# Kernel optimization log

Measured on AMD Instinct MI355X. Metric: run time of the kernel, lower is better.

Reference implementation:

```python
import jax, jax.numpy as jnp
import numpy as np

NUM_FILTER = 256
CAPS_LEN = 8
NUM_EMOTIONS = 8
OUT_DIM = 16
NUM_CHANNEL = 25
TIME_LEN = 25
NUM_CAPS = NUM_CHANNEL * TIME_LEN * (NUM_FILTER // CAPS_LEN)  # 20000
NUM_ITERATIONS = 3


def setup_inputs() -> dict:
    key = jax.random.key(0)
    ks = jax.random.split(key, 10)
    B = 32
    x = jax.random.normal(ks[0], (B, 54, 54), jnp.float32)
    conv1_w = jax.random.normal(ks[1], (NUM_FILTER, 1, 6, 6), jnp.float32) * 0.05
    conv1_b = jax.random.normal(ks[2], (NUM_FILTER,), jnp.float32) * 0.01
    conv2_w = jax.random.normal(ks[3], (NUM_FILTER, NUM_FILTER, 6, 6), jnp.float32) * 0.01
    conv2_b = jax.random.normal(ks[4], (NUM_FILTER,), jnp.float32) * 0.01
    conv3_w = jax.random.normal(ks[5], (NUM_FILTER, 2 * NUM_FILTER, 1, 1), jnp.float32) * 0.05
    conv3_b = jax.random.normal(ks[6], (NUM_FILTER,), jnp.float32) * 0.01
    # PrimaryCaps: one Linear(caps_len -> caps_len) per capsule, batched as [nc, out, in]
    pc_w = jax.random.normal(ks[7], (NUM_CAPS, CAPS_LEN, CAPS_LEN), jnp.float32) * 0.1
    pc_b = jax.random.normal(ks[8], (NUM_CAPS, CAPS_LEN), jnp.float32) * 0.1
    # EmotionCaps transform W: [nc, num_emotions, out_dim, in_dim]
    W = jax.random.normal(ks[9], (NUM_CAPS, NUM_EMOTIONS, OUT_DIM, CAPS_LEN), jnp.float32) * 0.05
    return {"x": x, "conv1_w": conv1_w, "conv1_b": conv1_b, "conv2_w": conv2_w,
            "conv2_b": conv2_b, "conv3_w": conv3_w, "conv3_b": conv3_b,
            "pc_w": pc_w, "pc_b": pc_b, "W": W}


def _conv(x, w, b, stride):
    y = jax.lax.conv_general_dilated(x, w, (stride, stride), 'VALID',
                                     dimension_numbers=('NCHW', 'OIHW', 'NCHW'))
    return y + b[None, :, None, None]


def _squash(s):
    # scale = |s|^2 / (1 + |s|^2); out = scale * s / (|s| + 1e-8)
    n2 = jnp.sum(s * s, axis=-1, keepdims=True)
    n = jnp.sqrt(n2)
    return (n2 / (1.0 + n2)) * s / (n + 1e-8)


def reference(x, conv1_w, conv1_b, conv2_w, conv2_b, conv3_w, conv3_b, pc_w, pc_b, W):
    x4 = x[:, None]                                    # [B,1,54,54]
    x1 = jax.nn.relu(_conv(x4, conv1_w, conv1_b, 2))   # [B,F,25,25]
    y = jnp.pad(x1, ((0, 0), (0, 0), (2, 3), (2, 3)))  # ZeroPad2d((2,3,2,3))
    y = jax.nn.relu(_conv(y, conv2_w, conv2_b, 1))     # [B,F,25,25]
    z = jax.nn.relu(jnp.concatenate([x1, y], axis=1))  # [B,2F,25,25]
    z = _conv(z, conv3_w, conv3_b, 1)                  # [B,F,25,25]
    B, F, H, Wd = z.shape
    # flatten to capsules: [B, F//caps_len, caps_len, H*W] -> [B, nc, caps_len]
    caps = z.reshape(B, F // CAPS_LEN, CAPS_LEN, H * Wd)
    caps = caps.transpose(0, 1, 3, 2).reshape(B, NUM_CAPS, CAPS_LEN)
    # PrimaryCaps: per-capsule linear, batched as a single einsum
    u = jnp.einsum('bni,noi->bno', caps, pc_w) + pc_b[None]   # [B,nc,caps_len]
    # EmotionCaps: u_hat[b,n,e,o] = W[n,e,o,i] u[b,n,i]
    u_hat = jnp.einsum('bni,neoi->bneo', u, W)                # [B,nc,ne,out_dim]
    b = jnp.zeros((B, NUM_CAPS, NUM_EMOTIONS), u.dtype)
    v = None
    for r in range(NUM_ITERATIONS):
        c = jax.nn.softmax(b, axis=2)[..., None]              # [B,nc,ne,1]
        v = _squash(jnp.sum(c * u_hat, axis=1))               # [B,ne,out_dim]
        if r < NUM_ITERATIONS - 1:
            b = b + jnp.einsum('bneo,beo->bne', u_hat, v)
    return jnp.linalg.norm(v, axis=-1)                        # [B,ne]
```

## Files before the change

### kernel.cpp

```cpp
#include <hip/hip_runtime.h>
#include <hip/hip_fp16.h>

typedef unsigned short u16;
typedef __attribute__((ext_vector_type(8))) short bf16x8;
typedef __attribute__((ext_vector_type(4))) float floatx4;
typedef __attribute__((ext_vector_type(2))) _Float16 half2v;

#define NPIX 625
#define NCAPS 20000
#define K2 9216

__device__ __forceinline__ u16 f2bf(float f) {
  unsigned u = __float_as_uint(f);
  return (u16)((u + 0x7fffu + ((u >> 16) & 1u)) >> 16);
}

__device__ __forceinline__ unsigned h16(float f) {
  union { _Float16 h; u16 b; } c;
  c.h = (_Float16)f;
  return (unsigned)c.b;
}

__device__ __forceinline__ half2v as_h2(unsigned u) {
  union { unsigned i; half2v h; } c;
  c.i = u;
  return c.h;
}

__device__ __forceinline__ float dot2f(unsigned a, unsigned b, float c) {
#if __has_builtin(__builtin_amdgcn_fdot2)
  return __builtin_amdgcn_fdot2(as_h2(a), as_h2(b), c, false);
#else
  half2v x = as_h2(a), y = as_h2(b);
  return fmaf((float)x[1], (float)y[1], fmaf((float)x[0], (float)y[0], c));
#endif
}

__device__ __forceinline__ float dotrow16(uint4 w, uint4 u) {
  float s = dot2f(w.x, u.x, 0.f);
  s = dot2f(w.y, u.y, s);
  s = dot2f(w.z, u.z, s);
  s = dot2f(w.w, u.w, s);
  return s;
}

__device__ __forceinline__ float dot8v(float4 a0, float4 a1, float4 b0, float4 b1) {
  float s = a0.x * b0.x;
  s = fmaf(a0.y, b0.y, s); s = fmaf(a0.z, b0.z, s); s = fmaf(a0.w, b0.w, s);
  s = fmaf(a1.x, b1.x, s); s = fmaf(a1.y, b1.y, s);
  s = fmaf(a1.z, b1.z, s); s = fmaf(a1.w, b1.w, s);
  return s;
}

#define GLDS16(g, l) __builtin_amdgcn_global_load_lds( \
    (const __attribute__((address_space(1))) void*)(g), \
    (__attribute__((address_space(3))) void*)(l), 16, 0, 0)

__global__ void prep_conv1(const float* __restrict__ w2, const float* __restrict__ w3,
                           u16* __restrict__ A2c, u16* __restrict__ A3,
                           const float* __restrict__ x, const float* __restrict__ w1,
                           const float* __restrict__ b1, u16* __restrict__ x1p) {
  if (blockIdx.x < 256) {
    const int oc = blockIdx.x, c = threadIdx.x;
    const float* src = w2 + (oc * 256 + c) * 36;
    float v[36];
#pragma unroll
    for (int k = 0; k < 9; k++) {
      const float4 q = *(const float4*)(src + k * 4);
      v[k * 4 + 0] = q.x; v[k * 4 + 1] = q.y; v[k * 4 + 2] = q.z; v[k * 4 + 3] = q.w;
    }
#pragma unroll
    for (int g = 0; g < 36; g++) {
      const int ktp = g / 9, tl = g % 9;
      A2c[(ktp * 256 + oc) * 2304 + tl * 256 + c] = f2bf(v[g]);
    }
  } else if (blockIdx.x < 384) {
    const int j = (blockIdx.x - 256) * 1024 + threadIdx.x * 4;
    const float4 q = *(const float4*)(w3 + j);
    ushort4 p;
    p.x = f2bf(q.x); p.y = f2bf(q.y); p.z = f2bf(q.z); p.w = f2bf(q.w);
    *(ushort4*)(A3 + j) = p;
  } else {
    const int blk = blockIdx.x - 384;
    const int b = blk / 25, i = blk % 25;
    const int f = threadIdx.x;
    float wreg[36];
#pragma unroll
    for (int k = 0; k < 36; k++) wreg[k] = w1[f * 36 + k];
    float bias = b1[f];
    const float* xb = x + b * 54 * 54 + (2 * i) * 54;
    for (int j = 0; j < 25; j++) {
      float acc = bias;
#pragma unroll
      for (int ki = 0; ki < 6; ki++)
#pragma unroll
        for (int kj = 0; kj < 6; kj++)
          acc = fmaf(xb[ki * 54 + 2 * j + kj], wreg[ki * 6 + kj], acc);
      x1p[(((b * 30 + i + 2) * 30) + (j + 2)) * 256 + f] = f2bf(fmaxf(acc, 0.f));
    }
  }
}

__global__ __launch_bounds__(512, 2) void conv2_gemm(const u16* __restrict__ A2n,
    const u16* __restrict__ x1p, u16* __restrict__ P) {
  __shared__ __align__(16) u16 lds[2][26624];
  const int tid = threadIdx.x;
  const int lane = tid & 63, wave = tid >> 6;
  const int ntile = blockIdx.x, kt = blockIdx.y;
  const int wm = wave & 3, wn = wave >> 2;
  const int lrow = lane & 15, kg = lane >> 4;
  const bool extra = (tid < 256);

  const int trow = tid >> 3;
  const int xoff = 8 * ((tid & 7) ^ (trow & 7));
  const u16* aSrc = A2n + (kt * 256 + trow) * 2304 + xoff;
  const int nb = ntile * 160;
  auto pixrow = [&](int r) {
    const int n = nb + r;
    const int b = n / NPIX, p = n % NPIX;
    const int i = p / 25, j = p % 25;
    return ((b * 30 + i) * 30 + j) * 256;
  };
  const u16* bSrc0 = x1p + pixrow(trow) + xoff;
  const u16* bSrc1 = x1p + pixrow(64 + trow) + xoff;
  const u16* bSrc2 = extra ? (x1p + pixrow(128 + trow) + xoff) : x1p;

  auto stage = [&](int bb, int t) {
    u16* Ab = &lds[bb][0];
    u16* Bb = &lds[bb][16384];
    const int g = kt * 9 + (t >> 2);
    const int boff = ((g / 6) * 30 + (g % 6)) * 256 + (t & 3) * 64;
    const u16* a = aSrc + t * 64;
#pragma unroll
    for (int i = 0; i < 4; i++)
      GLDS16(a + i * (64 * 2304), Ab + i * 4096 + tid * 8);
    GLDS16(bSrc0 + boff, Bb + tid * 8);
    GLDS16(bSrc1 + boff, Bb + 4096 + tid * 8);
    if (extra) GLDS16(bSrc2 + boff, Bb + 8192 + tid * 8);
  };

  floatx4 acc[4][5] = {};
  const int jx0 = 8 * (kg ^ (lrow & 7));
  const int jx1 = 8 * ((4 + kg) ^ (lrow & 7));
  const int arow = wm * 64 + lrow;
  const int brow = wn * 80 + lrow;

  stage(0, 0);
  for (int t = 0; t < 36; t++) {
    const int bb = t & 1;
    if (t < 35) {
      stage(bb ^ 1, t + 1);
      if (extra) asm volatile("s_waitcnt vmcnt(7)" ::: "memory");
      else       asm volatile("s_waitcnt vmcnt(6)" ::: "memory");
    } else {
      asm volatile("s_waitcnt vmcnt(0)" ::: "memory");
    }
    __builtin_amdgcn_s_barrier();
    asm volatile("" ::: "memory");
    const u16* Ab = &lds[bb][0];
    const u16* Bb = &lds[bb][16384];
    bf16x8 af0[4], b0[5], af1[4], b1r[5];
#pragma unroll
    for (int fm = 0; fm < 4; fm++) af0[fm] = *(const bf16x8*)(Ab + (arow + fm * 16) * 64 + jx0);
#pragma unroll
    for (int fn = 0; fn < 5; fn++) b0[fn] = *(const bf16x8*)(Bb + (brow + fn * 16) * 64 + jx0);
    __builtin_amdgcn_s_setprio(1);
#pragma unroll
    for (int fm = 0; fm < 4; fm++)
#pragma unroll
      for (int fn = 0; fn < 5; fn++)
        acc[fm][fn] = __builtin_amdgcn_mfma_f32_16x16x32_bf16(af0[fm], b0[fn], acc[fm][fn], 0, 0, 0);
    __builtin_amdgcn_s_setprio(0);
#pragma unroll
    for (int fm = 0; fm < 4; fm++) af1[fm] = *(const bf16x8*)(Ab + (arow + fm * 16) * 64 + jx1);
#pragma unroll
    for (int fn = 0; fn < 5; fn++) b1r[fn] = *(const bf16x8*)(Bb + (brow + fn * 16) * 64 + jx1);
    __builtin_amdgcn_s_setprio(1);
#pragma unroll
    for (int fm = 0; fm < 4; fm++)
#pragma unroll
      for (int fn = 0; fn < 5; fn++)
        acc[fm][fn] = __builtin_amdgcn_mfma_f32_16x16x32_bf16(af1[fm], b1r[fn], acc[fm][fn], 0, 0, 0);
    __builtin_amdgcn_s_setprio(0);
    asm volatile("" ::: "memory");
    __builtin_amdgcn_s_barrier();
  }

  u16* Pk = P + kt * 5120000;
#pragma unroll
  for (int fn = 0; fn < 5; fn++) {
    const int n = nb + wn * 80 + fn * 16 + lrow;
#pragma unroll
    for (int fm = 0; fm < 4; fm++) {
      const int oc = wm * 64 + fm * 16 + kg * 4;
      ushort4 pk;
      pk.x = f2bf(acc[fm][fn][0]);
      pk.y = f2bf(acc[fm][fn][1]);
      pk.z = f2bf(acc[fm][fn][2]);
      pk.w = f2bf(acc[fm][fn][3]);
      *(ushort4*)(Pk + n * 256 + oc) = pk;
    }
  }
}

__global__ void conv2_red(const u16* __restrict__ P, const float* __restrict__ bias2,
                          u16* __restrict__ y) {
  const int idx = blockIdx.x * 256 + threadIdx.x;
  const ushort4 p0 = *(const ushort4*)(P + idx * 4);
  const ushort4 p1 = *(const ushort4*)(P + 5120000 + idx * 4);
  const ushort4 p2 = *(const ushort4*)(P + 10240000 + idx * 4);
  const ushort4 p3 = *(const ushort4*)(P + 15360000 + idx * 4);
  const float4 bs = *(const float4*)(bias2 + ((idx * 4) & 255));
  auto bf = [](unsigned v) { return __uint_as_float(v << 16); };
  float sx = bf(p0.x) + bf(p1.x) + bf(p2.x) + bf(p3.x) + bs.x;
  float sy = bf(p0.y) + bf(p1.y) + bf(p2.y) + bf(p3.y) + bs.y;
  float sz = bf(p0.z) + bf(p1.z) + bf(p2.z) + bf(p3.z) + bs.z;
  float sw = bf(p0.w) + bf(p1.w) + bf(p2.w) + bf(p3.w) + bs.w;
  ushort4 pk;
  pk.x = f2bf(fmaxf(sx, 0.f));
  pk.y = f2bf(fmaxf(sy, 0.f));
  pk.z = f2bf(fmaxf(sz, 0.f));
  pk.w = f2bf(fmaxf(sw, 0.f));
  *(ushort4*)(y + idx * 4) = pk;
}

__global__ __launch_bounds__(256) void conv3_gemm(const u16* __restrict__ A3,
    const u16* __restrict__ x1p, const u16* __restrict__ y, u16* __restrict__ P3) {
  __shared__ u16 As[128 * 32];
  __shared__ u16 Bs[128 * 32];
  const int tid = threadIdx.x;
  const int lane = tid & 63, wave = tid >> 6;
  const int mtile = blockIdx.x, ntile = blockIdx.y, kt = blockIdx.z;

  const int seg0 = tid, seg1 = tid + 256;
  const u16* ga0 = A3 + (mtile * 128 + (seg0 >> 2)) * 512 + (seg0 & 3) * 8 + kt * 256;
  const u16* ga1 = A3 + (mtile * 128 + (seg1 >> 2)) * 512 + (seg1 & 3) * 8 + kt * 256;

  auto mkbase = [&](int seg) {
    int n = ntile * 128 + (seg >> 2);
    if (n > NCAPS - 1) n = NCAPS - 1;
    if (kt == 0) {
      int b = n / NPIX, p = n % NPIX;
      int i = p / 25, j = p % 25;
      return x1p + ((b * 30 + i + 2) * 30 + (j + 2)) * 256 + (seg & 3) * 8;
    }
    return y + n * 256 + (seg & 3) * 8;
  };
  const u16* gs0 = mkbase(seg0);
  const u16* gs1 = mkbase(seg1);

  floatx4 acc[4][4] = {};
  const int wm = wave & 1, wn = wave >> 1;
  const int lrow = lane & 15, kgrp = lane >> 4;

  for (int kc = 0; kc < 8; kc++) {
    GLDS16(ga0 + kc * 32, As + seg0 * 8);
    GLDS16(ga1 + kc * 32, As + seg1 * 8);
    GLDS16(gs0 + kc * 32, Bs + seg0 * 8);
    GLDS16(gs1 + kc * 32, Bs + seg1 * 8);
    __syncthreads();
    bf16x8 af[4], bfr[4];
#pragma unroll
    for (int tt = 0; tt < 4; tt++) {
      af[tt]  = *(const bf16x8*)(As + (wm * 64 + tt * 16 + lrow) * 32 + kgrp * 8);
      bfr[tt] = *(const bf16x8*)(Bs + (wn * 64 + tt * 16 + lrow) * 32 + kgrp * 8);
    }
#pragma unroll
    for (int tm = 0; tm < 4; tm++)
#pragma unroll
      for (int tn = 0; tn < 4; tn++)
        acc[tm][tn] = __builtin_amdgcn_mfma_f32_16x16x32_bf16(af[tm], bfr[tn], acc[tm][tn], 0, 0, 0);
    __syncthreads();
  }

  u16* Pk = P3 + kt * 5120000;
  const int nb = ntile * 128 + wn * 64;
  const int fb = mtile * 128 + wm * 64 + kgrp * 4;
#pragma unroll
  for (int tn = 0; tn < 4; tn++) {
    int n = nb + tn * 16 + lrow;
    if (n < NCAPS) {
#pragma unroll
      for (int tm = 0; tm < 4; tm++) {
        int f0 = fb + tm * 16;
        ushort4 pk;
        pk.x = f2bf(acc[tm][tn][0]);
        pk.y = f2bf(acc[tm][tn][1]);
        pk.z = f2bf(acc[tm][tn][2]);
        pk.w = f2bf(acc[tm][tn][3]);
        *(ushort4*)(Pk + n * 256 + f0) = pk;
      }
    }
  }
}

__global__ void prep_caps(const float* __restrict__ W, u16* __restrict__ Wbs,
                          const u16* __restrict__ P3, const float* __restrict__ b3,
                          const float* __restrict__ pcw, const float* __restrict__ pcb,
                          unsigned* __restrict__ u2) {
  const int tid = threadIdx.x;
  if (blockIdx.x < 10000) {
    int r = blockIdx.x * 256 + tid;
    int n = r >> 7, eo = r & 127;
    int e = eo >> 4, o = eo & 15;
    const float* src = W + n * 1024 + eo * 8;
    const float4 v0 = *(const float4*)src;
    const float4 v1 = *(const float4*)(src + 4);
    u16* dst = Wbs + n * 1088 + e * 136 + o * 8;
    ushort4 p0, p1;
    p0.x = (u16)h16(v0.x); p0.y = (u16)h16(v0.y); p0.z = (u16)h16(v0.z); p0.w = (u16)h16(v0.w);
    p1.x = (u16)h16(v1.x); p1.y = (u16)h16(v1.y); p1.z = (u16)h16(v1.z); p1.w = (u16)h16(v1.w);
    *(ushort4*)dst = p0;
    *(ushort4*)(dst + 4) = p1;
  } else {
    const int blk = blockIdx.x - 10000;
    const int b = tid >> 3, o = tid & 7;
    for (int k = 0; k < 8; k++) {
      const int n = blk * 8 + k;
      const int g = n / NPIX, p = n % NPIX;
      const u16* pa = P3 + ((b * NPIX + p) * 256 + g * 8);
      const uint4 qa = *(const uint4*)pa;
      const uint4 qb = *(const uint4*)(pa + 5120000);
      const float* bp = b3 + g * 8;
      const float4 bb0 = *(const float4*)bp;
      const float4 bb1 = *(const float4*)(bp + 4);
      float4 c0, c1;
      c0.x = __uint_as_float(qa.x << 16) + __uint_as_float(qb.x << 16) + bb0.x;
      c0.y = __uint_as_float(qa.x & 0xffff0000u) + __uint_as_float(qb.x & 0xffff0000u) + bb0.y;
      c0.z = __uint_as_float(qa.y << 16) + __uint_as_float(qb.y << 16) + bb0.z;
      c0.w = __uint_as_float(qa.y & 0xffff0000u) + __uint_as_float(qb.y & 0xffff0000u) + bb0.w;
      c1.x = __uint_as_float(qa.z << 16) + __uint_as_float(qb.z << 16) + bb1.x;
      c1.y = __uint_as_float(qa.z & 0xffff0000u) + __uint_as_float(qb.z & 0xffff0000u) + bb1.y;
      c1.z = __uint_as_float(qa.w << 16) + __uint_as_float(qb.w << 16) + bb1.z;
      c1.w = __uint_as_float(qa.w & 0xffff0000u) + __uint_as_float(qb.w & 0xffff0000u) + bb1.w;
      const float* pw = pcw + n * 64 + o * 8;
      float4 w0 = *(const float4*)pw;
      float4 w1 = *(const float4*)(pw + 4);
      const float myu = pcb[n * 8 + o] + dot8v(w0, w1, c0, c1);
      const float partner = __shfl_xor(myu, 1, 64);
      if (!(o & 1)) {
        unsigned pk = h16(myu) | (h16(partner) << 16);
        u2[n * 128 + b * 4 + (o >> 1)] = pk;
      }
    }
  }
}

__global__ __launch_bounds__(256, 4) void caps_accb2(const unsigned* __restrict__ u2,
    const u16* __restrict__ Wbs, const float* __restrict__ vsum,
    float* __restrict__ Spart, int zero_v) {
  __shared__ u16 Ws[16 * 1088];
  const int tid = threadIdx.x;
  const int b = tid >> 3, e = tid & 7;
  const int n0 = blockIdx.x * 16;

  const u16* gsrc = Wbs + n0 * 1088;
#pragma unroll
  for (int k = 0; k < 9; k++) {
    const int idx = k * 256 + tid;
    if (idx < 2176) GLDS16(gsrc + idx * 8, Ws + idx * 8);
  }

  float4 V0 = make_float4(0.f, 0.f, 0.f, 0.f), V1 = V0, V2 = V0, V3 = V0;
  if (!zero_v) {
    const float* vp = vsum + tid * 16;
    V0 = *(const float4*)vp;
    V1 = *(const float4*)(vp + 4);
    V2 = *(const float4*)(vp + 8);
    V3 = *(const float4*)(vp + 12);
  }
  float s0 = 0.f, s1 = 0.f, s2 = 0.f, s3 = 0.f, s4 = 0.f, s5 = 0.f, s6 = 0.f, s7 = 0.f;
  float s8 = 0.f, s9 = 0.f, s10 = 0.f, s11 = 0.f, s12 = 0.f, s13 = 0.f, s14 = 0.f, s15 = 0.f;

  __syncthreads();

  for (int it = 0; it < 16; it++) {
    const int n = n0 + it;
    const uint4 up = *(const uint4*)(u2 + n * 128 + b * 4);
    const u16* Wn = Ws + it * 1088 + e * 136;
    float h0, h1, h2, h3, h4, h5, h6, h7, h8, h9, h10, h11, h12, h13, h14, h15;
#define ROW(o, H) { uint4 w = *(const uint4*)(Wn + (o) * 8); H = dotrow16(w, up); }
    ROW(0, h0)   ROW(1, h1)   ROW(2, h2)   ROW(3, h3)
    ROW(4, h4)   ROW(5, h5)   ROW(6, h6)   ROW(7, h7)
    ROW(8, h8)   ROW(9, h9)   ROW(10, h10) ROW(11, h11)
    ROW(12, h12) ROW(13, h13) ROW(14, h14) ROW(15, h15)
#undef ROW
    float c;
    if (zero_v) {
      c = 0.125f;
    } else {
      float blog = h0 * V0.x;
      blog = fmaf(h1, V0.y, blog);  blog = fmaf(h2, V0.z, blog);  blog = fmaf(h3, V0.w, blog);
      blog = fmaf(h4, V1.x, blog);  blog = fmaf(h5, V1.y, blog);  blog = fmaf(h6, V1.z, blog);
      blog = fmaf(h7, V1.w, blog);  blog = fmaf(h8, V2.x, blog);  blog = fmaf(h9, V2.y, blog);
      blog = fmaf(h10, V2.z, blog); blog = fmaf(h11, V2.w, blog); blog = fmaf(h12, V3.x, blog);
      blog = fmaf(h13, V3.y, blog); blog = fmaf(h14, V3.z, blog); blog = fmaf(h15, V3.w, blog);
      float m = blog;
      m = fmaxf(m, __shfl_xor(m, 1, 64));
      m = fmaxf(m, __shfl_xor(m, 2, 64));
      m = fmaxf(m, __shfl_xor(m, 4, 64));
      float ex = __expf(blog - m);
      float ss = ex;
      ss += __shfl_xor(ss, 1, 64);
      ss += __shfl_xor(ss, 2, 64);
      ss += __shfl_xor(ss, 4, 64);
      c = ex / ss;
    }
    s0 = fmaf(c, h0, s0);   s1 = fmaf(c, h1, s1);   s2 = fmaf(c, h2, s2);   s3 = fmaf(c, h3, s3);
    s4 = fmaf(c, h4, s4);   s5 = fmaf(c, h5, s5);   s6 = fmaf(c, h6, s6);   s7 = fmaf(c, h7, s7);
    s8 = fmaf(c, h8, s8);   s9 = fmaf(c, h9, s9);   s10 = fmaf(c, h10, s10); s11 = fmaf(c, h11, s11);
    s12 = fmaf(c, h12, s12); s13 = fmaf(c, h13, s13); s14 = fmaf(c, h14, s14); s15 = fmaf(c, h15, s15);
  }
  float* Sp = Spart + blockIdx.x * 4096 + tid * 16;
  *(float4*)(Sp + 0)  = make_float4(s0, s1, s2, s3);
  *(float4*)(Sp + 4)  = make_float4(s4, s5, s6, s7);
  *(float4*)(Sp + 8)  = make_float4(s8, s9, s10, s11);
  *(float4*)(Sp + 12) = make_float4(s12, s13, s14, s15);
}

__global__ void caps_redB(const float* __restrict__ Spart, float* __restrict__ Sp2) {
  const int j = blockIdx.x * 256 + threadIdx.x;
  const int r0 = blockIdx.y * 50;
  float a0 = 0.f, a1 = 0.f;
  for (int r = 0; r < 50; r += 2) {
    a0 += Spart[(r0 + r) * 4096 + j];
    a1 += Spart[(r0 + r + 1) * 4096 + j];
  }
  Sp2[blockIdx.y * 4096 + j] = a0 + a1;
}

__global__ void caps_v2(const float* __restrict__ Sp2, float* __restrict__ vsum, int add) {
  const int t = threadIdx.x;
  float4 a0 = make_float4(0.f, 0.f, 0.f, 0.f), a1 = a0, a2 = a0, a3 = a0;
  for (int r = 0; r < 25; r++) {
    const float* sp = Sp2 + r * 4096 + t * 16;
    const float4 q0 = *(const float4*)sp;
    const float4 q1 = *(const float4*)(sp + 4);
    const float4 q2 = *(const float4*)(sp + 8);
    const float4 q3 = *(const float4*)(sp + 12);
    a0.x += q0.x; a0.y += q0.y; a0.z += q0.z; a0.w += q0.w;
    a1.x += q1.x; a1.y += q1.y; a1.z += q1.z; a1.w += q1.w;
    a2.x += q2.x; a2.y += q2.y; a2.z += q2.z; a2.w += q2.w;
    a3.x += q3.x; a3.y += q3.y; a3.z += q3.z; a3.w += q3.w;
  }
  float n2 = a0.x * a0.x;
  n2 = fmaf(a0.y, a0.y, n2); n2 = fmaf(a0.z, a0.z, n2); n2 = fmaf(a0.w, a0.w, n2);
  n2 = fmaf(a1.x, a1.x, n2); n2 = fmaf(a1.y, a1.y, n2); n2 = fmaf(a1.z, a1.z, n2); n2 = fmaf(a1.w, a1.w, n2);
  n2 = fmaf(a2.x, a2.x, n2); n2 = fmaf(a2.y, a2.y, n2); n2 = fmaf(a2.z, a2.z, n2); n2 = fmaf(a2.w, a2.w, n2);
  n2 = fmaf(a3.x, a3.x, n2); n2 = fmaf(a3.y, a3.y, n2); n2 = fmaf(a3.z, a3.z, n2); n2 = fmaf(a3.w, a3.w, n2);
  const float n = sqrtf(n2);
  const float scale = n2 / ((1.f + n2) * (n + 1e-8f));
  float* vp = vsum + t * 16;
  float4 o0, o1, o2, o3;
  if (add) {
    o0 = *(float4*)(vp + 0); o1 = *(float4*)(vp + 4); o2 = *(float4*)(vp + 8); o3 = *(float4*)(vp + 12);
  } else {
    o0 = make_float4(0.f, 0.f, 0.f, 0.f); o1 = o0; o2 = o0; o3 = o0;
  }
  o0.x = fmaf(a0.x, scale, o0.x); o0.y = fmaf(a0.y, scale, o0.y);
  o0.z = fmaf(a0.z, scale, o0.z); o0.w = fmaf(a0.w, scale, o0.w);
  o1.x = fmaf(a1.x, scale, o1.x); o1.y = fmaf(a1.y, scale, o1.y);
  o1.z = fmaf(a1.z, scale, o1.z); o1.w = fmaf(a1.w, scale, o1.w);
  o2.x = fmaf(a2.x, scale, o2.x); o2.y = fmaf(a2.y, scale, o2.y);
  o2.z = fmaf(a2.z, scale, o2.z); o2.w = fmaf(a2.w, scale, o2.w);
  o3.x = fmaf(a3.x, scale, o3.x); o3.y = fmaf(a3.y, scale, o3.y);
  o3.z = fmaf(a3.z, scale, o3.z); o3.w = fmaf(a3.w, scale, o3.w);
  *(float4*)(vp + 0) = o0; *(float4*)(vp + 4) = o1;
  *(float4*)(vp + 8) = o2; *(float4*)(vp + 12) = o3;
}

__global__ void caps_out2(const float* __restrict__ Sp2, float* __restrict__ out) {
  const int t = threadIdx.x;
  float4 a0 = make_float4(0.f, 0.f, 0.f, 0.f), a1 = a0, a2 = a0, a3 = a0;
  for (int r = 0; r < 25; r++) {
    const float* sp = Sp2 + r * 4096 + t * 16;
    const float4 q0 = *(const float4*)sp;
    const float4 q1 = *(const float4*)(sp + 4);
    const float4 q2 = *(const float4*)(sp + 8);
    const float4 q3 = *(const float4*)(sp + 12);
    a0.x += q0.x; a0.y += q0.y; a0.z += q0.z; a0.w += q0.w;
    a1.x += q1.x; a1.y += q1.y; a1.z += q1.z; a1.w += q1.w;
    a2.x += q2.x; a2.y += q2.y; a2.z += q2.z; a2.w += q2.w;
    a3.x += q3.x; a3.y += q3.y; a3.z += q3.z; a3.w += q3.w;
  }
  float n2 = a0.x * a0.x;
  n2 = fmaf(a0.y, a0.y, n2); n2 = fmaf(a0.z, a0.z, n2); n2 = fmaf(a0.w, a0.w, n2);
  n2 = fmaf(a1.x, a1.x, n2); n2 = fmaf(a1.y, a1.y, n2); n2 = fmaf(a1.z, a1.z, n2); n2 = fmaf(a1.w, a1.w, n2);
  n2 = fmaf(a2.x, a2.x, n2); n2 = fmaf(a2.y, a2.y, n2); n2 = fmaf(a2.z, a2.z, n2); n2 = fmaf(a2.w, a2.w, n2);
  n2 = fmaf(a3.x, a3.x, n2); n2 = fmaf(a3.y, a3.y, n2); n2 = fmaf(a3.z, a3.z, n2); n2 = fmaf(a3.w, a3.w, n2);
  const float n = sqrtf(n2);
  out[t] = n * n2 / ((1.f + n2) * (n + 1e-8f));
}

extern "C" void kernel_launch(void* const* d_in, const int* in_sizes, int n_in,
                              void* d_out, int out_size, void* d_ws, size_t ws_size,
                              hipStream_t stream) {
  const float* x   = (const float*)d_in[0];
  const float* w1  = (const float*)d_in[1];
  const float* b1  = (const float*)d_in[2];
  const float* w2  = (const float*)d_in[3];
  const float* b2  = (const float*)d_in[4];
  const float* w3  = (const float*)d_in[5];
  const float* b3  = (const float*)d_in[6];
  const float* pcw = (const float*)d_in[7];
  const float* pcb = (const float*)d_in[8];
  const float* W   = (const float*)d_in[9];
  float* out = (float*)d_out;

  char* ws = (char*)d_ws;

  u16*   x1p = (u16*)(ws + 0);
  u16*   A2  = (u16*)(ws + 14745600);
  u16*   A3  = (u16*)(ws + 19464192);
  u16*   y   = (u16*)(ws + 19726336);
  u16*   P   = (u16*)(ws + 29966336);
  u16*   P3  = (u16*)(ws + 43520000);
  u16*   Wbs = (u16*)(ws + 0);
  float* Spart = (float*)(ws + 43520000);
  unsigned* u2 = (unsigned*)(ws + 64000000);
  float* Sp2 = (float*)(ws + 74240000);
  float* vs  = (float*)(ws + 74649600);

  hipMemsetAsync(x1p, 0, 14745600, stream);

  prep_conv1<<<1184, 256, 0, stream>>>(w2, w3, A2, A3, x, w1, b1, x1p);
  conv2_gemm<<<dim3(125, 4), 512, 0, stream>>>(A2, x1p, P);
  conv2_red<<<5000, 256, 0, stream>>>(P, b2, y);
  conv3_gemm<<<dim3(2, 157, 2), 256, 0, stream>>>(A3, x1p, y, P3);
  prep_caps<<<12500, 256, 0, stream>>>(W, Wbs, P3, b3, pcw, pcb, u2);

  for (int pass = 0; pass < 3; pass++) {
    caps_accb2<<<1250, 256, 0, stream>>>(u2, Wbs, vs, Spart, pass == 0 ? 1 : 0);
    caps_redB<<<dim3(16, 25), 256, 0, stream>>>(Spart, Sp2);
    if (pass == 0)      caps_v2<<<1, 256, 0, stream>>>(Sp2, vs, 0);
    else if (pass == 1) caps_v2<<<1, 256, 0, stream>>>(Sp2, vs, 1);
    else                caps_out2<<<1, 256, 0, stream>>>(Sp2, out);
  }
}
```

Baseline: 454.0 us.

## Triple-buffer conv2 GEMM LDS with depth-2 prefetch interleaved across MFMA phases

The conv2 implicit-GEMM kernel moves from double to triple LDS buffering, so global-to-LDS loads run two k-steps ahead instead of one. Each k-step is split into four MFMA sub-phases, and the prefetch loads are spread across them, separated by block barriers and sched_barriers. The aim is to hide global memory latency and shorten the per-step register live range by loading fewer fragments at a time. In exchange, the kernel uses about 156 KB of LDS and launch bounds drop to one block per CU. Each iteration now has several more barriers, which may cost synchronization time.

```diff
diff --git a/kernel.cpp b/kernel.cpp
--- a/kernel.cpp
+++ b/kernel.cpp
@@ -55,6 +55,8 @@
 #define GLDS16(g, l) __builtin_amdgcn_global_load_lds( \
     (const __attribute__((address_space(1))) void*)(g), \
     (__attribute__((address_space(3))) void*)(l), 16, 0, 0)
+
+#define MFMA16(a, b, c) __builtin_amdgcn_mfma_f32_16x16x32_bf16((a), (b), (c), 0, 0, 0)
 
 __global__ void prep_conv1(const float* __restrict__ w2, const float* __restrict__ w3,
                            u16* __restrict__ A2c, u16* __restrict__ A3,
@@ -101,9 +103,9 @@
   }
 }
 
-__global__ __launch_bounds__(512, 2) void conv2_gemm(const u16* __restrict__ A2n,
+__global__ __launch_bounds__(512, 1) void conv2_gemm(const u16* __restrict__ A2n,
     const u16* __restrict__ x1p, u16* __restrict__ P) {
-  __shared__ __align__(16) u16 lds[2][26624];
+  __shared__ __align__(16) u16 lds[3][26624];
   const int tid = threadIdx.x;
   const int lane = tid & 63, wave = tid >> 6;
   const int ntile = blockIdx.x, kt = blockIdx.y;
@@ -125,18 +127,9 @@
   const u16* bSrc1 = x1p + pixrow(64 + trow) + xoff;
   const u16* bSrc2 = extra ? (x1p + pixrow(128 + trow) + xoff) : x1p;
 
-  auto stage = [&](int bb, int t) {
-    u16* Ab = &lds[bb][0];
-    u16* Bb = &lds[bb][16384];
+  auto boffOf = [&](int t) {
     const int g = kt * 9 + (t >> 2);
-    const int boff = ((g / 6) * 30 + (g % 6)) * 256 + (t & 3) * 64;
-    const u16* a = aSrc + t * 64;
-#pragma unroll
-    for (int i = 0; i < 4; i++)
-      GLDS16(a + i * (64 * 2304), Ab + i * 4096 + tid * 8);
-    GLDS16(bSrc0 + boff, Bb + tid * 8);
-    GLDS16(bSrc1 + boff, Bb + 4096 + tid * 8);
-    if (extra) GLDS16(bSrc2 + boff, Bb + 8192 + tid * 8);
+    return ((g / 6) * 30 + (g % 6)) * 256 + (t & 3) * 64;
   };
 
   floatx4 acc[4][5] = {};
@@ -145,45 +138,108 @@
   const int arow = wm * 64 + lrow;
   const int brow = wn * 80 + lrow;
 
-  stage(0, 0);
+#pragma unroll
+  for (int pt = 0; pt < 2; pt++) {
+    u16* L = lds[pt];
+    const u16* a = aSrc + pt * 64;
+    GLDS16(a,              L + tid * 8);
+    GLDS16(a + 64 * 2304,  L + 4096 + tid * 8);
+    GLDS16(a + 128 * 2304, L + 8192 + tid * 8);
+    GLDS16(a + 192 * 2304, L + 12288 + tid * 8);
+    const int bo = boffOf(pt);
+    GLDS16(bSrc0 + bo, L + 16384 + tid * 8);
+    GLDS16(bSrc1 + bo, L + 20480 + tid * 8);
+    if (extra) GLDS16(bSrc2 + bo, L + 24576 + tid * 8);
+  }
+
+  int bb = 0;
   for (int t = 0; t < 36; t++) {
-    const int bb = t & 1;
+    u16* Cur = lds[bb];
+    int pb = bb + 2; if (pb >= 3) pb -= 3;
+    u16* Pre = lds[pb];
+    const bool st = (t < 34);
+    const u16* aPre = aSrc + (t + 2) * 64;
+    const int boPre = st ? boffOf(t + 2) : 0;
+
     if (t < 35) {
-      stage(bb ^ 1, t + 1);
       if (extra) asm volatile("s_waitcnt vmcnt(7)" ::: "memory");
       else       asm volatile("s_waitcnt vmcnt(6)" ::: "memory");
     } else {
       asm volatile("s_waitcnt vmcnt(0)" ::: "memory");
     }
-    __builtin_amdgcn_s_barrier();
-    asm volatile("" ::: "memory");
-    const u16* Ab = &lds[bb][0];
-    const u16* Bb = &lds[bb][16384];
-    bf16x8 af0[4], b0[5], af1[4], b1r[5];
-#pragma unroll
-    for (int fm = 0; fm < 4; fm++) af0[fm] = *(const bf16x8*)(Ab + (arow + fm * 16) * 64 + jx0);
-#pragma unroll
-    for (int fn = 0; fn < 5; fn++) b0[fn] = *(const bf16x8*)(Bb + (brow + fn * 16) * 64 + jx0);
+    if (st) {
+      GLDS16(aPre,             Pre + tid * 8);
+      GLDS16(aPre + 64 * 2304, Pre + 4096 + tid * 8);
+    }
+    __builtin_amdgcn_s_barrier();
+    bf16x8 a0 = *(const bf16x8*)(Cur + (arow +  0) * 64 + jx0);
+    bf16x8 a1 = *(const bf16x8*)(Cur + (arow + 16) * 64 + jx0);
+    bf16x8 bA[5];
+#pragma unroll
+    for (int fn = 0; fn < 5; fn++)
+      bA[fn] = *(const bf16x8*)(Cur + 16384 + (brow + fn * 16) * 64 + jx0);
     __builtin_amdgcn_s_setprio(1);
 #pragma unroll
-    for (int fm = 0; fm < 4; fm++)
-#pragma unroll
-      for (int fn = 0; fn < 5; fn++)
-        acc[fm][fn] = __builtin_amdgcn_mfma_f32_16x16x32_bf16(af0[fm], b0[fn], acc[fm][fn], 0, 0, 0);
+    for (int fn = 0; fn < 5; fn++) {
+      acc[0][fn] = MFMA16(a0, bA[fn], acc[0][fn]);
+      acc[1][fn] = MFMA16(a1, bA[fn], acc[1][fn]);
+    }
     __builtin_amdgcn_s_setprio(0);
-#pragma unroll
-    for (int fm = 0; fm < 4; fm++) af1[fm] = *(const bf16x8*)(Ab + (arow + fm * 16) * 64 + jx1);
-#pragma unroll
-    for (int fn = 0; fn < 5; fn++) b1r[fn] = *(const bf16x8*)(Bb + (brow + fn * 16) * 64 + jx1);
+    __builtin_amdgcn_sched_barrier(0);
+    __builtin_amdgcn_s_barrier();
+
+    bf16x8 a2 = *(const bf16x8*)(Cur + (arow + 32) * 64 + jx0);
+    bf16x8 a3 = *(const bf16x8*)(Cur + (arow + 48) * 64 + jx0);
+    if (st) {
+      GLDS16(aPre + 128 * 2304, Pre + 8192 + tid * 8);
+      GLDS16(aPre + 192 * 2304, Pre + 12288 + tid * 8);
+    }
+    __builtin_amdgcn_s_barrier();
     __builtin_amdgcn_s_setprio(1);
 #pragma unroll
-    for (int fm = 0; fm < 4; fm++)
-#pragma unroll
-      for (int fn = 0; fn < 5; fn++)
-        acc[fm][fn] = __builtin_amdgcn_mfma_f32_16x16x32_bf16(af1[fm], b1r[fn], acc[fm][fn], 0, 0, 0);
+    for (int fn = 0; fn < 5; fn++) {
+      acc[2][fn] = MFMA16(a2, bA[fn], acc[2][fn]);
+      acc[3][fn] = MFMA16(a3, bA[fn], acc[3][fn]);
+    }
     __builtin_amdgcn_s_setprio(0);
-    asm volatile("" ::: "memory");
-    __builtin_amdgcn_s_barrier();
+    __builtin_amdgcn_sched_barrier(0);
+    __builtin_amdgcn_s_barrier();
+
+    a0 = *(const bf16x8*)(Cur + (arow +  0) * 64 + jx1);
+    a1 = *(const bf16x8*)(Cur + (arow + 16) * 64 + jx1);
+#pragma unroll
+    for (int fn = 0; fn < 5; fn++)
+      bA[fn] = *(const bf16x8*)(Cur + 16384 + (brow + fn * 16) * 64 + jx1);
+    if (st) {
+      GLDS16(bSrc0 + boPre, Pre + 16384 + tid * 8);
+      GLDS16(bSrc1 + boPre, Pre + 20480 + tid * 8);
+    }
+    __builtin_amdgcn_s_barrier();
+    __builtin_amdgcn_s_setprio(1);
+#pragma unroll
+    for (int fn = 0; fn < 5; fn++) {
+      acc[0][fn] = MFMA16(a0, bA[fn], acc[0][fn]);
+      acc[1][fn] = MFMA16(a1, bA[fn], acc[1][fn]);
+    }
+    __builtin_amdgcn_s_setprio(0);
+    __builtin_amdgcn_sched_barrier(0);
+    __builtin_amdgcn_s_barrier();
+
+    a2 = *(const bf16x8*)(Cur + (arow + 32) * 64 + jx1);
+    a3 = *(const bf16x8*)(Cur + (arow + 48) * 64 + jx1);
+    if (st && extra) GLDS16(bSrc2 + boPre, Pre + 24576 + tid * 8);
+    __builtin_amdgcn_s_barrier();
+    __builtin_amdgcn_s_setprio(1);
+#pragma unroll
+    for (int fn = 0; fn < 5; fn++) {
+      acc[2][fn] = MFMA16(a2, bA[fn], acc[2][fn]);
+      acc[3][fn] = MFMA16(a3, bA[fn], acc[3][fn]);
+    }
+    __builtin_amdgcn_s_setprio(0);
+    __builtin_amdgcn_sched_barrier(0);
+    __builtin_amdgcn_s_barrier();
+
+    bb++; if (bb == 3) bb = 0;
   }
 
   u16* Pk = P + kt * 5120000;
```

Result: no change. 448.8 us (-1.1%).

## Enlarge conv2 GEMM tile to 256x320 with interleaved staging schedule

Applied to the files above, without the earlier changes.

The conv2 implicit-GEMM block tile doubles along N, from 160 to 320 pixels, so each block now covers all 256 output channels. Each wave computes a 128x80 sub-tile with 40 accumulators, and the grid shrinks to 63x4 blocks. The global-to-LDS staging for the next k-step is split into A and B halves and interleaved between MFMA phases behind barriers and sched_barriers, to overlap loads with compute and raise operand reuse per byte loaded. In exchange, occupancy drops to one block per CU because of the larger LDS and register footprint. The grid is also only 252 blocks, which risks underfilling the GPU and tail effects, and the last tile needs clamping.

```diff
diff --git a/kernel.cpp b/kernel.cpp
--- a/kernel.cpp
+++ b/kernel.cpp
@@ -55,6 +55,8 @@
 #define GLDS16(g, l) __builtin_amdgcn_global_load_lds( \
     (const __attribute__((address_space(1))) void*)(g), \
     (__attribute__((address_space(3))) void*)(l), 16, 0, 0)
+
+#define MFMA16(a, b, c) __builtin_amdgcn_mfma_f32_16x16x32_bf16((a), (b), (c), 0, 0, 0)
 
 __global__ void prep_conv1(const float* __restrict__ w2, const float* __restrict__ w3,
                            u16* __restrict__ A2c, u16* __restrict__ A3,
@@ -101,88 +103,135 @@
   }
 }
 
-__global__ __launch_bounds__(512, 2) void conv2_gemm(const u16* __restrict__ A2n,
+__global__ __launch_bounds__(512, 1) void conv2_gemm(const u16* __restrict__ A2n,
     const u16* __restrict__ x1p, u16* __restrict__ P) {
-  __shared__ __align__(16) u16 lds[2][26624];
+  __shared__ __align__(16) u16 lds[2][36864];
   const int tid = threadIdx.x;
   const int lane = tid & 63, wave = tid >> 6;
   const int ntile = blockIdx.x, kt = blockIdx.y;
-  const int wm = wave & 3, wn = wave >> 2;
+  const int wm = wave & 1, wn = wave >> 1;
   const int lrow = lane & 15, kg = lane >> 4;
-  const bool extra = (tid < 256);
 
   const int trow = tid >> 3;
   const int xoff = 8 * ((tid & 7) ^ (trow & 7));
   const u16* aSrc = A2n + (kt * 256 + trow) * 2304 + xoff;
-  const int nb = ntile * 160;
+  const int nb = ntile * 320;
   auto pixrow = [&](int r) {
-    const int n = nb + r;
+    int n = nb + r;
+    if (n > NCAPS - 1) n = NCAPS - 1;
     const int b = n / NPIX, p = n % NPIX;
     const int i = p / 25, j = p % 25;
     return ((b * 30 + i) * 30 + j) * 256;
   };
   const u16* bSrc0 = x1p + pixrow(trow) + xoff;
   const u16* bSrc1 = x1p + pixrow(64 + trow) + xoff;
-  const u16* bSrc2 = extra ? (x1p + pixrow(128 + trow) + xoff) : x1p;
-
-  auto stage = [&](int bb, int t) {
-    u16* Ab = &lds[bb][0];
-    u16* Bb = &lds[bb][16384];
-    const int g = kt * 9 + (t >> 2);
-    const int boff = ((g / 6) * 30 + (g % 6)) * 256 + (t & 3) * 64;
-    const u16* a = aSrc + t * 64;
-#pragma unroll
-    for (int i = 0; i < 4; i++)
-      GLDS16(a + i * (64 * 2304), Ab + i * 4096 + tid * 8);
-    GLDS16(bSrc0 + boff, Bb + tid * 8);
-    GLDS16(bSrc1 + boff, Bb + 4096 + tid * 8);
-    if (extra) GLDS16(bSrc2 + boff, Bb + 8192 + tid * 8);
+  const u16* bSrc2 = x1p + pixrow(128 + trow) + xoff;
+  const u16* bSrc3 = x1p + pixrow(192 + trow) + xoff;
+  const u16* bSrc4 = x1p + pixrow(256 + trow) + xoff;
+
+  auto stageA = [&](u16* L, int tt) {
+    const u16* a = aSrc + tt * 64;
+    GLDS16(a,               L + tid * 8);
+    GLDS16(a + 64 * 2304,   L + 4096 + tid * 8);
+    GLDS16(a + 128 * 2304,  L + 8192 + tid * 8);
+    GLDS16(a + 192 * 2304,  L + 12288 + tid * 8);
   };
-
-  floatx4 acc[4][5] = {};
+  auto stageB = [&](u16* L, int tt) {
+    const int g = kt * 9 + (tt >> 2);
+    const int boff = ((g / 6) * 30 + (g % 6)) * 256 + (tt & 3) * 64;
+    GLDS16(bSrc0 + boff, L + 16384 + tid * 8);
+    GLDS16(bSrc1 + boff, L + 20480 + tid * 8);
+    GLDS16(bSrc2 + boff, L + 24576 + tid * 8);
+    GLDS16(bSrc3 + boff, L + 28672 + tid * 8);
+    GLDS16(bSrc4 + boff, L + 32768 + tid * 8);
+  };
+
+  floatx4 acc[8][5] = {};
   const int jx0 = 8 * (kg ^ (lrow & 7));
   const int jx1 = 8 * ((4 + kg) ^ (lrow & 7));
-  const int arow = wm * 64 + lrow;
+  const int arow = wm * 128 + lrow;
   const int brow = wn * 80 + lrow;
 
-  stage(0, 0);
+  stageA(lds[0], 0);
+  stageB(lds[0], 0);
+  asm volatile("s_waitcnt vmcnt(0)" ::: "memory");
+  __builtin_amdgcn_s_barrier();
+
   for (int t = 0; t < 36; t++) {
-    const int bb = t & 1;
-    if (t < 35) {
-      stage(bb ^ 1, t + 1);
-      if (extra) asm volatile("s_waitcnt vmcnt(7)" ::: "memory");
-      else       asm volatile("s_waitcnt vmcnt(6)" ::: "memory");
-    } else {
-      asm volatile("s_waitcnt vmcnt(0)" ::: "memory");
-    }
-    __builtin_amdgcn_s_barrier();
+    u16* Cur = lds[t & 1];
+    u16* Oth = lds[(t & 1) ^ 1];
+    const bool st = (t < 35);
+    bf16x8 af[4], bv[5];
+
+#pragma unroll
+    for (int fm = 0; fm < 4; fm++)
+      af[fm] = *(const bf16x8*)(Cur + (arow + fm * 16) * 64 + jx0);
+#pragma unroll
+    for (int fn = 0; fn < 5; fn++)
+      bv[fn] = *(const bf16x8*)(Cur + 16384 + (brow + fn * 16) * 64 + jx0);
+    if (st) stageA(Oth, t + 1);
     asm volatile("" ::: "memory");
-    const u16* Ab = &lds[bb][0];
-    const u16* Bb = &lds[bb][16384];
-    bf16x8 af0[4], b0[5], af1[4], b1r[5];
-#pragma unroll
-    for (int fm = 0; fm < 4; fm++) af0[fm] = *(const bf16x8*)(Ab + (arow + fm * 16) * 64 + jx0);
-#pragma unroll
-    for (int fn = 0; fn < 5; fn++) b0[fn] = *(const bf16x8*)(Bb + (brow + fn * 16) * 64 + jx0);
+    __builtin_amdgcn_s_barrier();
     __builtin_amdgcn_s_setprio(1);
 #pragma unroll
     for (int fm = 0; fm < 4; fm++)
 #pragma unroll
       for (int fn = 0; fn < 5; fn++)
-        acc[fm][fn] = __builtin_amdgcn_mfma_f32_16x16x32_bf16(af0[fm], b0[fn], acc[fm][fn], 0, 0, 0);
+        acc[fm][fn] = MFMA16(af[fm], bv[fn], acc[fm][fn]);
     __builtin_amdgcn_s_setprio(0);
-#pragma unroll
-    for (int fm = 0; fm < 4; fm++) af1[fm] = *(const bf16x8*)(Ab + (arow + fm * 16) * 64 + jx1);
-#pragma unroll
-    for (int fn = 0; fn < 5; fn++) b1r[fn] = *(const bf16x8*)(Bb + (brow + fn * 16) * 64 + jx1);
+    __builtin_amdgcn_sched_barrier(0);
+    __builtin_amdgcn_s_barrier();
+
+    bf16x8 ag[4];
+#pragma unroll
+    for (int fm = 0; fm < 4; fm++)
+      ag[fm] = *(const bf16x8*)(Cur + (arow + 64 + fm * 16) * 64 + jx0);
+    if (st) stageB(Oth, t + 1);
+    asm volatile("" ::: "memory");
+    __builtin_amdgcn_s_barrier();
     __builtin_amdgcn_s_setprio(1);
 #pragma unroll
     for (int fm = 0; fm < 4; fm++)
 #pragma unroll
       for (int fn = 0; fn < 5; fn++)
-        acc[fm][fn] = __builtin_amdgcn_mfma_f32_16x16x32_bf16(af1[fm], b1r[fn], acc[fm][fn], 0, 0, 0);
+        acc[4 + fm][fn] = MFMA16(ag[fm], bv[fn], acc[4 + fm][fn]);
     __builtin_amdgcn_s_setprio(0);
+    __builtin_amdgcn_sched_barrier(0);
+    __builtin_amdgcn_s_barrier();
+
+#pragma unroll
+    for (int fm = 0; fm < 4; fm++)
+      af[fm] = *(const bf16x8*)(Cur + (arow + fm * 16) * 64 + jx1);
+#pragma unroll
+    for (int fn = 0; fn < 5; fn++)
+      bv[fn] = *(const bf16x8*)(Cur + 16384 + (brow + fn * 16) * 64 + jx1);
     asm volatile("" ::: "memory");
+    __builtin_amdgcn_s_barrier();
+    __builtin_amdgcn_s_setprio(1);
+#pragma unroll
+    for (int fm = 0; fm < 4; fm++)
+#pragma unroll
+      for (int fn = 0; fn < 5; fn++)
+        acc[fm][fn] = MFMA16(af[fm], bv[fn], acc[fm][fn]);
+    __builtin_amdgcn_s_setprio(0);
+    __builtin_amdgcn_sched_barrier(0);
+    __builtin_amdgcn_s_barrier();
+
+#pragma unroll
+    for (int fm = 0; fm < 4; fm++)
+      ag[fm] = *(const bf16x8*)(Cur + (arow + 64 + fm * 16) * 64 + jx1);
+    asm volatile("" ::: "memory");
+    __builtin_amdgcn_s_barrier();
+    __builtin_amdgcn_s_setprio(1);
+#pragma unroll
+    for (int fm = 0; fm < 4; fm++)
+#pragma unroll
+      for (int fn = 0; fn < 5; fn++)
+        acc[4 + fm][fn] = MFMA16(ag[fm], bv[fn], acc[4 + fm][fn]);
+    __builtin_amdgcn_s_setprio(0);
+    __builtin_amdgcn_sched_barrier(0);
+    asm volatile("s_waitcnt vmcnt(0)" ::: "memory");
+    __builtin_amdgcn_sched_barrier(0);
     __builtin_amdgcn_s_barrier();
   }
 
@@ -190,15 +239,17 @@
 #pragma unroll
   for (int fn = 0; fn < 5; fn++) {
     const int n = nb + wn * 80 + fn * 16 + lrow;
-#pragma unroll
-    for (int fm = 0; fm < 4; fm++) {
-      const int oc = wm * 64 + fm * 16 + kg * 4;
-      ushort4 pk;
-      pk.x = f2bf(acc[fm][fn][0]);
-      pk.y = f2bf(acc[fm][fn][1]);
-      pk.z = f2bf(acc[fm][fn][2]);
-      pk.w = f2bf(acc[fm][fn][3]);
-      *(ushort4*)(Pk + n * 256 + oc) = pk;
+    if (n < NCAPS) {
+#pragma unroll
+      for (int fm = 0; fm < 8; fm++) {
+        const int oc = wm * 128 + fm * 16 + kg * 4;
+        ushort4 pk;
+        pk.x = f2bf(acc[fm][fn][0]);
+        pk.y = f2bf(acc[fm][fn][1]);
+        pk.z = f2bf(acc[fm][fn][2]);
+        pk.w = f2bf(acc[fm][fn][3]);
+        *(ushort4*)(Pk + n * 256 + oc) = pk;
+      }
     }
   }
 }
@@ -524,7 +575,7 @@
   hipMemsetAsync(x1p, 0, 14745600, stream);
 
   prep_conv1<<<1184, 256, 0, stream>>>(w2, w3, A2, A3, x, w1, b1, x1p);
-  conv2_gemm<<<dim3(125, 4), 512, 0, stream>>>(A2, x1p, P);
+  conv2_gemm<<<dim3(63, 4), 512, 0, stream>>>(A2, x1p, P);
   conv2_red<<<5000, 256, 0, stream>>>(P, b2, y);
   conv3_gemm<<<dim3(2, 157, 2), 256, 0, stream>>>(A3, x1p, y, P3);
   prep_caps<<<12500, 256, 0, stream>>>(W, Wbs, P3, b3, pcw, pcb, u2);
```

New measurement: 441.0 us. 1.03x faster.
